# Optimization experiments

Hardware: AMD Instinct MI355X
Metric: run time of the kernel (lower is better)

## Reference

```python
import jax, jax.numpy as jnp
import numpy as np

B, S, E, H = 2, 2048, 1024, 16
D = E // H  # head_dim = 64


def setup_inputs() -> dict:
    key = jax.random.key(0)
    ks = jax.random.split(key, 6)
    scale = 1.0 / np.sqrt(E)
    x = jax.random.normal(ks[0], (B, S, E), dtype=jnp.float32)
    mask = jnp.ones((B, S), dtype=jnp.int32)
    Wqkv = jax.random.normal(ks[1], (E, 3 * E), dtype=jnp.float32) * scale
    bqkv = jax.random.normal(ks[2], (3 * E,), dtype=jnp.float32) * 0.01
    Wout = jax.random.normal(ks[3], (E, E), dtype=jnp.float32) * scale
    bout = jax.random.normal(ks[4], (E,), dtype=jnp.float32) * 0.01
    return {"x": x, "mask": mask, "Wqkv": Wqkv, "bqkv": bqkv, "Wout": Wout, "bout": bout}


def reference(x, mask, Wqkv, bqkv, Wout, bout):
    Bn, Sn, En = x.shape
    qkv = x @ Wqkv + bqkv                      # [B,S,3E]
    qkv = qkv.reshape(Bn, Sn, 3, H, D)
    qkv = jnp.transpose(qkv, (2, 0, 3, 1, 4))  # [3,B,H,S,D]
    q, k, v = qkv[0], qkv[1], qkv[2]
    scores = jnp.einsum('bhqd,bhkd->bhqk', q, k) / np.sqrt(D).astype(np.float32)
    m = mask[:, None, None, :]                 # [B,1,1,S]
    scores = jnp.where(m == 0, jnp.float32(-jnp.inf), scores)
    attn = jax.nn.softmax(scores, axis=-1)
    out = jnp.einsum('bhqk,bhkd->bhqd', attn, v)  # [B,H,S,D]
    out = jnp.transpose(out, (0, 2, 1, 3)).reshape(Bn, Sn, En)
    return out @ Wout + bout
```

## Files before the change

kernel.cpp:

```cpp
#include <hip/hip_runtime.h>


typedef __attribute__((ext_vector_type(8))) short short8;
typedef __attribute__((ext_vector_type(4))) short short4b;
typedef __attribute__((ext_vector_type(4))) float floatx4;
typedef unsigned short ushort_t;

static __device__ __forceinline__ ushort_t f2bf(float f) {
    unsigned u = __float_as_uint(f);
    u += 0x7fffu + ((u >> 16) & 1u);
    return (ushort_t)(u >> 16);
}
static __device__ __forceinline__ float bf2f(ushort_t h) {
    return __uint_as_float(((unsigned)h) << 16);
}
#if __has_builtin(__builtin_amdgcn_cvt_pk_bf16_f32)
typedef __attribute__((ext_vector_type(2))) __bf16 bf16x2_t;
static __device__ __forceinline__ unsigned pack2bf(float a, float b) {
    bf16x2_t r = __builtin_amdgcn_cvt_pk_bf16_f32(a, b);
    return __builtin_bit_cast(unsigned, r);
}
#else
static __device__ __forceinline__ unsigned pack2bf(float a, float b) {
    return (unsigned)f2bf(a) | ((unsigned)f2bf(b) << 16);
}
#endif
static __device__ __forceinline__ float hexp2(float x) {
    return __builtin_amdgcn_exp2f(x);
}
static __device__ __forceinline__ void gload16(const void* g, void* l) {
    __builtin_amdgcn_global_load_lds(
        (const __attribute__((address_space(1))) unsigned int*)g,
        (__attribute__((address_space(3))) unsigned int*)l, 16, 0, 0);
}

static __device__ __forceinline__ floatx4 mfma16(short4b a, short4b b, floatx4 c) {
#if __has_builtin(__builtin_amdgcn_mfma_f32_16x16x16_bf16)
    return __builtin_amdgcn_mfma_f32_16x16x16_bf16(a, b, c, 0, 0, 0);
#elif __has_builtin(__builtin_amdgcn_mfma_f32_16x16x16bf16_1k)
    return __builtin_amdgcn_mfma_f32_16x16x16bf16_1k(a, b, c, 0, 0, 0);
#else
    asm("v_mfma_f32_16x16x16_bf16 %0, %1, %2, %0" : "+v"(c) : "v"(a), "v"(b));
    return c;
#endif
}

__global__ __launch_bounds__(256) void prep(
    const float* __restrict__ x, ushort_t* __restrict__ xb,
    const float* __restrict__ Wqkv, ushort_t* __restrict__ wqT,
    const float* __restrict__ Wout, ushort_t* __restrict__ woT,
    const int* __restrict__ mask, float* __restrict__ maddg)
{
    __shared__ float tile[32][33];
    const int bk = blockIdx.x;
    const int t = threadIdx.x;
    if (bk < 4096) {
        int i = bk * 256 + t;
        float4 v = ((const float4*)x)[i];
        uint2 o;
        o.x = pack2bf(v.x, v.y);
        o.y = pack2bf(v.z, v.w);
        ((uint2*)xb)[i] = o;
        return;
    }
    if (bk < 8192) {
        const float* W; ushort_t* WT; int K, N, id;
        if (bk < 7168) { W = Wqkv; WT = wqT; K = 1024; N = 3072; id = bk - 4096;
                         int nb = (id % 96) * 32, kb = (id / 96) * 32;
                         const int r = t >> 3, c4 = (t & 7) * 4;
                         float4 v = *(const float4*)&W[(size_t)(kb + r) * N + nb + c4];
                         tile[r][c4+0]=v.x; tile[r][c4+1]=v.y; tile[r][c4+2]=v.z; tile[r][c4+3]=v.w;
                         __syncthreads();
                         uint2 o;
                         o.x = pack2bf(tile[c4+0][r], tile[c4+1][r]);
                         o.y = pack2bf(tile[c4+2][r], tile[c4+3][r]);
                         ((uint2*)WT)[((size_t)(nb + r) * K + kb + c4) >> 2] = o;
        } else {         W = Wout; WT = woT; K = 1024; N = 1024; id = bk - 7168;
                         int nb = (id % 32) * 32, kb = (id / 32) * 32;
                         const int r = t >> 3, c4 = (t & 7) * 4;
                         float4 v = *(const float4*)&W[(size_t)(kb + r) * N + nb + c4];
                         tile[r][c4+0]=v.x; tile[r][c4+1]=v.y; tile[r][c4+2]=v.z; tile[r][c4+3]=v.w;
                         __syncthreads();
                         uint2 o;
                         o.x = pack2bf(tile[c4+0][r], tile[c4+1][r]);
                         o.y = pack2bf(tile[c4+2][r], tile[c4+3][r]);
                         ((uint2*)WT)[((size_t)(nb + r) * K + kb + c4) >> 2] = o;
        }
        return;
    }
    {
        int i = (bk - 8192) * 256 + t;
        maddg[i] = (mask[i] ? 0.f : -1e30f) - 24.0f;
    }
}

__global__ __launch_bounds__(256, 3) void gemm_qkv(
    const ushort_t* __restrict__ A, const ushort_t* __restrict__ B,
    const float* __restrict__ bias, ushort_t* __restrict__ qkvb,
    ushort_t* __restrict__ vtg)
{
    const int K = 1024;
    __shared__ ushort_t Ah[128][32], Bh[128][32];
    __shared__ ushort_t Tb[64][136];
    const int bn = blockIdx.x * 128, bm = blockIdx.y * 128;
    const int t = threadIdx.x, w = t >> 6, lane = t & 63;
    const int l15 = lane & 15, quad = lane >> 4;
    const int wm = w >> 1, wn = w & 1;

    const int srow = w * 32 + (lane >> 2);
    const int skp  = (lane & 3) ^ ((lane >> 2) & 3);
    const int scol = skp * 8;
    const ushort_t* ga = A + (size_t)(bm + srow) * K + scol;
    const ushort_t* gb = B + (size_t)(bn + srow) * K + scol;
    const size_t rstep = (size_t)16 * K;
    const int fcol = ((quad ^ (l15 & 3)) * 8);

    floatx4 acc[4][4];
    #pragma unroll
    for (int mt = 0; mt < 4; ++mt)
        #pragma unroll
        for (int nt = 0; nt < 4; ++nt) acc[mt][nt] = (floatx4){0.f, 0.f, 0.f, 0.f};

    for (int k0 = 0; k0 < K; k0 += 32) {
        #pragma unroll
        for (int i = 0; i < 2; ++i) {
            gload16(ga + i * rstep + k0, &Ah[w * 32 + i * 16][0]);
            gload16(gb + i * rstep + k0, &Bh[w * 32 + i * 16][0]);
        }
        __syncthreads();
        short8 ah[4], bh[4];
        #pragma unroll
        for (int x = 0; x < 4; ++x) {
            ah[x] = *(const short8*)&Ah[wm * 64 + x * 16 + l15][fcol];
            bh[x] = *(const short8*)&Bh[wn * 64 + x * 16 + l15][fcol];
        }
        #pragma unroll
        for (int mt = 0; mt < 4; ++mt)
            #pragma unroll
            for (int nt = 0; nt < 4; ++nt)
                acc[mt][nt] = __builtin_amdgcn_mfma_f32_16x16x32_bf16(ah[mt], bh[nt], acc[mt][nt], 0, 0, 0);
        __syncthreads();
    }

    if (bn < 2048) {
        #pragma unroll
        for (int mt = 0; mt < 4; ++mt)
            #pragma unroll
            for (int r = 0; r < 4; ++r) {
                size_t row = (size_t)(bm + wm * 64 + mt * 16 + quad * 4 + r) * 2048;
                #pragma unroll
                for (int nt = 0; nt < 4; ++nt) {
                    int col = bn + wn * 64 + nt * 16 + l15;
                    qkvb[row + col] = f2bf(acc[mt][nt][r] + bias[col]);
                }
            }
    } else {
        const int h0 = (bn - 2048) >> 6;
        const int b  = bm >> 11, s0 = bm & 2047;
        #pragma unroll
        for (int hh = 0; hh < 2; ++hh) {
            if (wn == hh) {
                #pragma unroll
                for (int mt = 0; mt < 4; ++mt)
                    #pragma unroll
                    for (int nt = 0; nt < 4; ++nt) {
                        int d = nt * 16 + l15;
                        int sb = wm * 64 + mt * 16 + quad * 4;
                        float bv = bias[bn + hh * 64 + nt * 16 + l15];
                        uint2 pk;
                        pk.x = pack2bf(acc[mt][nt][0] + bv, acc[mt][nt][1] + bv);
                        pk.y = pack2bf(acc[mt][nt][2] + bv, acc[mt][nt][3] + bv);
                        *(uint2*)&Tb[d][sb] = pk;
                    }
            }
            __syncthreads();
            ushort_t* vbase = vtg + ((size_t)((b * 16 + h0 + hh) * 64)) * 2048 + s0;
            #pragma unroll
            for (int it = 0; it < 4; ++it) {
                int idx = t + it * 256;
                int d = idx >> 4, ch = idx & 15;
                uint4 v = *(const uint4*)&Tb[d][ch * 8];
                *(uint4*)&vbase[(size_t)d * 2048 + ch * 8] = v;
            }
            __syncthreads();
        }
    }
}

__global__ __launch_bounds__(256, 3) void gemm_bf16_f32_64(
    const ushort_t* __restrict__ A, const ushort_t* __restrict__ B,
    const float* __restrict__ bias, float* __restrict__ C,
    int M, int N, int K)
{
    __shared__ ushort_t Ah[64][32], Bh[128][32];
    const int bn = blockIdx.x * 128, bm = blockIdx.y * 64;
    const int t = threadIdx.x, w = t >> 6, lane = t & 63;
    const int l15 = lane & 15, quad = lane >> 4;
    const int wm = w >> 1, wn = w & 1;

    const int srow = w * 16 + (lane >> 2);
    const int skp  = (lane & 3) ^ ((lane >> 2) & 3);
    const int scol = skp * 8;
    const ushort_t* ga  = A + (size_t)(bm + srow) * K + scol;
    const ushort_t* gb0 = B + (size_t)(bn + srow) * K + scol;
    const ushort_t* gb1 = B + (size_t)(bn + 64 + srow) * K + scol;
    const int fcol = ((quad ^ (l15 & 3)) * 8);

    floatx4 acc[2][4];
    #pragma unroll
    for (int mt = 0; mt < 2; ++mt)
        #pragma unroll
        for (int nt = 0; nt < 4; ++nt) acc[mt][nt] = (floatx4){0.f, 0.f, 0.f, 0.f};

    for (int k0 = 0; k0 < K; k0 += 32) {
        gload16(ga  + k0, &Ah[w * 16][0]);
        gload16(gb0 + k0, &Bh[w * 16][0]);
        gload16(gb1 + k0, &Bh[64 + w * 16][0]);
        __syncthreads();
        short8 ah[2], bh[4];
        #pragma unroll
        for (int x = 0; x < 2; ++x)
            ah[x] = *(const short8*)&Ah[wm * 32 + x * 16 + l15][fcol];
        #pragma unroll
        for (int x = 0; x < 4; ++x)
            bh[x] = *(const short8*)&Bh[wn * 64 + x * 16 + l15][fcol];
        #pragma unroll
        for (int mt = 0; mt < 2; ++mt)
            #pragma unroll
            for (int nt = 0; nt < 4; ++nt)
                acc[mt][nt] = __builtin_amdgcn_mfma_f32_16x16x32_bf16(ah[mt], bh[nt], acc[mt][nt], 0, 0, 0);
        __syncthreads();
    }
    #pragma unroll
    for (int mt = 0; mt < 2; ++mt)
        #pragma unroll
        for (int r = 0; r < 4; ++r) {
            size_t row = (size_t)(bm + wm * 32 + mt * 16 + quad * 4 + r) * N;
            #pragma unroll
            for (int nt = 0; nt < 4; ++nt) {
                int col = bn + wn * 64 + nt * 16 + l15;
                C[row + col] = acc[mt][nt][r] + bias[col];
            }
        }
}

__global__ __launch_bounds__(512, 4) void flash_v8(
    const ushort_t* __restrict__ qkv, const ushort_t* __restrict__ vtg,
    const float* __restrict__ maddg, ushort_t* __restrict__ attn)
{
    __shared__ ushort_t Ks[2][64][64];
    __shared__ ushort_t Vt[2][64][64];

    const int blk = blockIdx.x;
    const int xcd = blk & 7, rr = blk >> 3;
    const int qi = rr & 15, g = xcd + 8 * (rr >> 4);
    const int b = g >> 4, h = g & 15, q0 = qi * 128;

    const int t = threadIdx.x, wave = t >> 6, lane = t & 63;
    const int l15 = lane & 15, quad = lane >> 4;
    const size_t bS = (size_t)b * 2048;
    const float c1 = 0.125f * 1.44269504088896340736f;

    short8 qf[2];
    {
        int q = q0 + wave * 16 + l15;
        const ushort_t* qp = qkv + (bS + q) * 2048 + h * 64;
        qf[0] = *(const short8*)(qp + quad * 8);
        qf[1] = *(const short8*)(qp + 32 + quad * 8);
    }

    const int srow  = wave * 8 + (lane >> 3);
    const int schnk = ((lane & 7) ^ ((lane >> 3) & 7)) * 8;
    const ushort_t* gK = qkv + (bS + srow) * 2048 + 1024 + h * 64 + schnk;
    const ushort_t* gV = vtg + ((size_t)(b * 16 + h) * 64 + srow) * 2048 + schnk;
    const float* gM = maddg + b * 2048;

    gload16(gK, &Ks[0][wave * 8][0]);
    gload16(gV, &Vt[0][wave * 8][0]);
    __syncthreads();

    floatx4 outacc[4];
    float lsum = 0.f;
    #pragma unroll
    for (int dt = 0; dt < 4; ++dt) outacc[dt] = (floatx4){0.f, 0.f, 0.f, 0.f};

    int cur = 0;
    for (int kt = 0; kt < 32; ++kt) {
        const int k0 = kt * 64;
        {
            const int kn = (kt + 1 < 32) ? (kt + 1) * 64 : 0;
            const int nb = cur ^ 1;
            gload16(gK + (size_t)kn * 2048, &Ks[nb][wave * 8][0]);
            gload16(gV + kn,                &Vt[nb][wave * 8][0]);
        }
        float4 madd4[4];
        #pragma unroll
        for (int c = 0; c < 4; ++c)
            madd4[c] = *(const float4*)&gM[k0 + c * 16 + quad * 4];

        short8 kf[2][4];
        #pragma unroll
        for (int kc = 0; kc < 2; ++kc)
            #pragma unroll
            for (int c = 0; c < 4; ++c) {
                int ch = ((kc * 4 + quad) ^ (l15 & 7)) * 8;
                kf[kc][c] = *(const short8*)&Ks[cur][c * 16 + l15][ch];
            }
        short4b vA[4][4];
        #pragma unroll
        for (int c = 0; c < 4; ++c) {
            const int vby = (((2 * c + (quad >> 1)) ^ (l15 & 7)) * 16 + (quad & 1) * 8);
            #pragma unroll
            for (int dt = 0; dt < 4; ++dt)
                vA[c][dt] = *(const short4b*)((const char*)&Vt[cur][dt * 16 + l15][0] + vby);
        }

        floatx4 sc[4];
        __builtin_amdgcn_s_setprio(1);
        #pragma unroll
        for (int c = 0; c < 4; ++c) {
            sc[c] = (floatx4){0.f, 0.f, 0.f, 0.f};
            sc[c] = __builtin_amdgcn_mfma_f32_16x16x32_bf16(kf[0][c], qf[0], sc[c], 0, 0, 0);
            sc[c] = __builtin_amdgcn_mfma_f32_16x16x32_bf16(kf[1][c], qf[1], sc[c], 0, 0, 0);
        }
        __builtin_amdgcn_s_setprio(0);
        #pragma unroll
        for (int c = 0; c < 4; ++c) {
            float p0 = hexp2(fmaf(sc[c][0], c1, madd4[c].x));
            float p1 = hexp2(fmaf(sc[c][1], c1, madd4[c].y));
            float p2 = hexp2(fmaf(sc[c][2], c1, madd4[c].z));
            float p3 = hexp2(fmaf(sc[c][3], c1, madd4[c].w));
            lsum += (p0 + p1) + (p2 + p3);
            uint2 u;
            u.x = pack2bf(p0, p1);
            u.y = pack2bf(p2, p3);
            short4b pb = __builtin_bit_cast(short4b, u);
            __builtin_amdgcn_s_setprio(1);
            #pragma unroll
            for (int dt = 0; dt < 4; ++dt)
                outacc[dt] = mfma16(vA[c][dt], pb, outacc[dt]);
            __builtin_amdgcn_s_setprio(0);
        }
        __syncthreads();
        cur ^= 1;
    }

    {
        lsum += __shfl_xor(lsum, 16);
        lsum += __shfl_xor(lsum, 32);
        float inv = 1.f / lsum;
        int q = q0 + wave * 16 + l15;
        ushort_t* orow = attn + (bS + q) * 1024 + h * 64;
        #pragma unroll
        for (int dt = 0; dt < 4; ++dt) {
            uint2 pk;
            pk.x = pack2bf(outacc[dt][0] * inv, outacc[dt][1] * inv);
            pk.y = pack2bf(outacc[dt][2] * inv, outacc[dt][3] * inv);
            *(uint2*)&orow[dt * 16 + quad * 4] = pk;
        }
    }
}

extern "C" void kernel_launch(void* const* d_in, const int* in_sizes, int n_in,
                              void* d_out, int out_size, void* d_ws, size_t ws_size,
                              hipStream_t stream) {
    const float* x    = (const float*)d_in[0];
    const int*   mask = (const int*)  d_in[1];
    const float* Wqkv = (const float*)d_in[2];
    const float* bqkv = (const float*)d_in[3];
    const float* Wout = (const float*)d_in[4];
    const float* bout = (const float*)d_in[5];
    float* out = (float*)d_out;

    char* ws = (char*)d_ws;
    ushort_t* xb    = (ushort_t*)(ws);
    ushort_t* wqT   = (ushort_t*)(ws + 8388608);
    ushort_t* qkvb  = (ushort_t*)(ws + 14680064);
    ushort_t* vtg   = (ushort_t*)(ws + 31457280);
    ushort_t* attnb = (ushort_t*)(ws + 39845888);
    ushort_t* woT   = (ushort_t*)(ws + 48234496);
    float*    maddg = (float*)   (ws + 50331648);

    const int M = 4096, E = 1024, N3 = 3072;

    prep<<<dim3(8208), dim3(256), 0, stream>>>(
        x, xb, Wqkv, wqT, Wout, woT, mask, maddg);

    gemm_qkv<<<dim3(N3 / 128, M / 128), dim3(256), 0, stream>>>(
        xb, wqT, bqkv, qkvb, vtg);

    flash_v8<<<dim3(512), dim3(512), 0, stream>>>(qkvb, vtg, maddg, attnb);

    gemm_bf16_f32_64<<<dim3(E / 128, M / 64), dim3(256), 0, stream>>>(
        attnb, woT, bout, out, M, E, E);
}
```

Measured before the change: 196.8 us.

## Switch flash attention to 32x32x16 MFMA with permlane32 swap for P operand

The attention kernel now uses 32x32x16 bf16 MFMA tiles for both QK^T and PV. Each wave handles 32 queries instead of 16, and the block shrinks from 512 to 256 threads. The score fragments are rearranged into the B-operand layout with permlane32_swap, avoiding an LDS round-trip. K/V fragments are read from LDS inside the MFMA loops rather than preloaded. The larger MFMA tiles should cut instruction count and LDS traffic per FLOP, at the cost of more registers per wave and fewer waves per block.

```diff
diff --git a/kernel.cpp b/kernel.cpp
--- a/kernel.cpp
+++ b/kernel.cpp
@@ -4,6 +4,7 @@
 typedef __attribute__((ext_vector_type(8))) short short8;
 typedef __attribute__((ext_vector_type(4))) short short4b;
 typedef __attribute__((ext_vector_type(4))) float floatx4;
+typedef __attribute__((ext_vector_type(16))) float floatx16;
 typedef unsigned short ushort_t;
 
 static __device__ __forceinline__ ushort_t f2bf(float f) {
@@ -34,16 +35,24 @@
         (__attribute__((address_space(3))) unsigned int*)l, 16, 0, 0);
 }
 
-static __device__ __forceinline__ floatx4 mfma16(short4b a, short4b b, floatx4 c) {
-#if __has_builtin(__builtin_amdgcn_mfma_f32_16x16x16_bf16)
-    return __builtin_amdgcn_mfma_f32_16x16x16_bf16(a, b, c, 0, 0, 0);
-#elif __has_builtin(__builtin_amdgcn_mfma_f32_16x16x16bf16_1k)
-    return __builtin_amdgcn_mfma_f32_16x16x16bf16_1k(a, b, c, 0, 0, 0);
+#if __has_builtin(__builtin_amdgcn_permlane32_swap)
+typedef __attribute__((ext_vector_type(2))) unsigned uint2v_t;
+static __device__ __forceinline__ void plswap(unsigned x, unsigned y,
+                                              unsigned& o0, unsigned& o1) {
+    uint2v_t r = __builtin_amdgcn_permlane32_swap(x, y, false, false);
+    o0 = r.x; o1 = r.y;
+}
 #else
-    asm("v_mfma_f32_16x16x16_bf16 %0, %1, %2, %0" : "+v"(c) : "v"(a), "v"(b));
-    return c;
+static __device__ __forceinline__ void plswap(unsigned x, unsigned y,
+                                              unsigned& o0, unsigned& o1) {
+    int l = (int)(threadIdx.x & 63);
+    bool hi = l >= 32;
+    unsigned xsw = (unsigned)__shfl((int)x, l ^ 32);
+    unsigned ysw = (unsigned)__shfl((int)y, l ^ 32);
+    o0 = hi ? ysw : x;
+    o1 = hi ? y : xsw;
+}
 #endif
-}
 
 __global__ __launch_bounds__(256) void prep(
     const float* __restrict__ x, ushort_t* __restrict__ xb,
@@ -244,7 +253,7 @@
         }
 }
 
-__global__ __launch_bounds__(512, 4) void flash_v8(
+__global__ __launch_bounds__(256, 2) void flash_v10(
     const ushort_t* __restrict__ qkv, const ushort_t* __restrict__ vtg,
     const float* __restrict__ maddg, ushort_t* __restrict__ attn)
 {
@@ -257,32 +266,33 @@
     const int b = g >> 4, h = g & 15, q0 = qi * 128;
 
     const int t = threadIdx.x, wave = t >> 6, lane = t & 63;
-    const int l15 = lane & 15, quad = lane >> 4;
+    const int l31 = lane & 31, hi = lane >> 5, l7 = lane & 7;
     const size_t bS = (size_t)b * 2048;
     const float c1 = 0.125f * 1.44269504088896340736f;
 
-    short8 qf[2];
+    short8 qf[4];
     {
-        int q = q0 + wave * 16 + l15;
-        const ushort_t* qp = qkv + (bS + q) * 2048 + h * 64;
-        qf[0] = *(const short8*)(qp + quad * 8);
-        qf[1] = *(const short8*)(qp + 32 + quad * 8);
-    }
-
-    const int srow  = wave * 8 + (lane >> 3);
+        int q = q0 + wave * 32 + l31;
+        const ushort_t* qp = qkv + (bS + q) * 2048 + h * 64 + hi * 8;
+        #pragma unroll
+        for (int ks = 0; ks < 4; ++ks)
+            qf[ks] = *(const short8*)(qp + ks * 16);
+    }
+
+    const int srow  = wave * 16 + (lane >> 3);
     const int schnk = ((lane & 7) ^ ((lane >> 3) & 7)) * 8;
     const ushort_t* gK = qkv + (bS + srow) * 2048 + 1024 + h * 64 + schnk;
     const ushort_t* gV = vtg + ((size_t)(b * 16 + h) * 64 + srow) * 2048 + schnk;
     const float* gM = maddg + b * 2048;
 
-    gload16(gK, &Ks[0][wave * 8][0]);
-    gload16(gV, &Vt[0][wave * 8][0]);
+    gload16(gK,            &Ks[0][wave * 16][0]);
+    gload16(gK + 8 * 2048, &Ks[0][wave * 16 + 8][0]);
+    gload16(gV,            &Vt[0][wave * 16][0]);
+    gload16(gV + 8 * 2048, &Vt[0][wave * 16 + 8][0]);
     __syncthreads();
 
-    floatx4 outacc[4];
+    floatx16 outacc[2] = {};
     float lsum = 0.f;
-    #pragma unroll
-    for (int dt = 0; dt < 4; ++dt) outacc[dt] = (floatx4){0.f, 0.f, 0.f, 0.f};
 
     int cur = 0;
     for (int kt = 0; kt < 32; ++kt) {
@@ -290,55 +300,59 @@
         {
             const int kn = (kt + 1 < 32) ? (kt + 1) * 64 : 0;
             const int nb = cur ^ 1;
-            gload16(gK + (size_t)kn * 2048, &Ks[nb][wave * 8][0]);
-            gload16(gV + kn,                &Vt[nb][wave * 8][0]);
-        }
-        float4 madd4[4];
-        #pragma unroll
-        for (int c = 0; c < 4; ++c)
-            madd4[c] = *(const float4*)&gM[k0 + c * 16 + quad * 4];
-
-        short8 kf[2][4];
-        #pragma unroll
-        for (int kc = 0; kc < 2; ++kc)
-            #pragma unroll
-            for (int c = 0; c < 4; ++c) {
-                int ch = ((kc * 4 + quad) ^ (l15 & 7)) * 8;
-                kf[kc][c] = *(const short8*)&Ks[cur][c * 16 + l15][ch];
-            }
-        short4b vA[4][4];
-        #pragma unroll
-        for (int c = 0; c < 4; ++c) {
-            const int vby = (((2 * c + (quad >> 1)) ^ (l15 & 7)) * 16 + (quad & 1) * 8);
-            #pragma unroll
-            for (int dt = 0; dt < 4; ++dt)
-                vA[c][dt] = *(const short4b*)((const char*)&Vt[cur][dt * 16 + l15][0] + vby);
-        }
-
-        floatx4 sc[4];
+            gload16(gK + (size_t)kn * 2048,       &Ks[nb][wave * 16][0]);
+            gload16(gK + (size_t)(kn + 8) * 2048, &Ks[nb][wave * 16 + 8][0]);
+            gload16(gV + kn,                      &Vt[nb][wave * 16][0]);
+            gload16(gV + kn + 8 * 2048,           &Vt[nb][wave * 16 + 8][0]);
+        }
+        float4 m4[2][4];
+        #pragma unroll
+        for (int t32 = 0; t32 < 2; ++t32)
+            #pragma unroll
+            for (int gr = 0; gr < 4; ++gr)
+                m4[t32][gr] = *(const float4*)&gM[k0 + t32 * 32 + gr * 8 + hi * 4];
+
+        floatx16 sc[2] = {};
         __builtin_amdgcn_s_setprio(1);
         #pragma unroll
-        for (int c = 0; c < 4; ++c) {
-            sc[c] = (floatx4){0.f, 0.f, 0.f, 0.f};
-            sc[c] = __builtin_amdgcn_mfma_f32_16x16x32_bf16(kf[0][c], qf[0], sc[c], 0, 0, 0);
-            sc[c] = __builtin_amdgcn_mfma_f32_16x16x32_bf16(kf[1][c], qf[1], sc[c], 0, 0, 0);
-        }
+        for (int t32 = 0; t32 < 2; ++t32)
+            #pragma unroll
+            for (int ks = 0; ks < 4; ++ks) {
+                const int ch = ((2 * ks + hi) ^ l7) * 8;
+                short8 ka = *(const short8*)&Ks[cur][t32 * 32 + l31][ch];
+                sc[t32] = __builtin_amdgcn_mfma_f32_32x32x16_bf16(ka, qf[ks], sc[t32], 0, 0, 0);
+            }
         __builtin_amdgcn_s_setprio(0);
-        #pragma unroll
-        for (int c = 0; c < 4; ++c) {
-            float p0 = hexp2(fmaf(sc[c][0], c1, madd4[c].x));
-            float p1 = hexp2(fmaf(sc[c][1], c1, madd4[c].y));
-            float p2 = hexp2(fmaf(sc[c][2], c1, madd4[c].z));
-            float p3 = hexp2(fmaf(sc[c][3], c1, madd4[c].w));
-            lsum += (p0 + p1) + (p2 + p3);
-            uint2 u;
-            u.x = pack2bf(p0, p1);
-            u.y = pack2bf(p2, p3);
-            short4b pb = __builtin_bit_cast(short4b, u);
+
+        unsigned W[2][4][2];
+        #pragma unroll
+        for (int t32 = 0; t32 < 2; ++t32)
+            #pragma unroll
+            for (int gr = 0; gr < 4; ++gr) {
+                float p0 = hexp2(fmaf(sc[t32][gr * 4 + 0], c1, m4[t32][gr].x));
+                float p1 = hexp2(fmaf(sc[t32][gr * 4 + 1], c1, m4[t32][gr].y));
+                float p2 = hexp2(fmaf(sc[t32][gr * 4 + 2], c1, m4[t32][gr].z));
+                float p3 = hexp2(fmaf(sc[t32][gr * 4 + 3], c1, m4[t32][gr].w));
+                lsum += (p0 + p1) + (p2 + p3);
+                W[t32][gr][0] = pack2bf(p0, p1);
+                W[t32][gr][1] = pack2bf(p2, p3);
+            }
+
+        #pragma unroll
+        for (int ks2 = 0; ks2 < 4; ++ks2) {
+            const int t32 = ks2 >> 1;
+            const int ae  = (ks2 & 1) * 2;
+            uint4 u;
+            plswap(W[t32][ae][0], W[t32][ae + 1][0], u.x, u.z);
+            plswap(W[t32][ae][1], W[t32][ae + 1][1], u.y, u.w);
+            short8 pb = __builtin_bit_cast(short8, u);
+            const int ch = ((2 * ks2 + hi) ^ l7) * 8;
             __builtin_amdgcn_s_setprio(1);
             #pragma unroll
-            for (int dt = 0; dt < 4; ++dt)
-                outacc[dt] = mfma16(vA[c][dt], pb, outacc[dt]);
+            for (int dt = 0; dt < 2; ++dt) {
+                short8 va = *(const short8*)&Vt[cur][dt * 32 + l31][ch];
+                outacc[dt] = __builtin_amdgcn_mfma_f32_32x32x16_bf16(va, pb, outacc[dt], 0, 0, 0);
+            }
             __builtin_amdgcn_s_setprio(0);
         }
         __syncthreads();
@@ -346,18 +360,19 @@
     }
 
     {
-        lsum += __shfl_xor(lsum, 16);
         lsum += __shfl_xor(lsum, 32);
         float inv = 1.f / lsum;
-        int q = q0 + wave * 16 + l15;
+        int q = q0 + wave * 32 + l31;
         ushort_t* orow = attn + (bS + q) * 1024 + h * 64;
         #pragma unroll
-        for (int dt = 0; dt < 4; ++dt) {
-            uint2 pk;
-            pk.x = pack2bf(outacc[dt][0] * inv, outacc[dt][1] * inv);
-            pk.y = pack2bf(outacc[dt][2] * inv, outacc[dt][3] * inv);
-            *(uint2*)&orow[dt * 16 + quad * 4] = pk;
-        }
+        for (int dt = 0; dt < 2; ++dt)
+            #pragma unroll
+            for (int gr = 0; gr < 4; ++gr) {
+                uint2 pk;
+                pk.x = pack2bf(outacc[dt][gr * 4 + 0] * inv, outacc[dt][gr * 4 + 1] * inv);
+                pk.y = pack2bf(outacc[dt][gr * 4 + 2] * inv, outacc[dt][gr * 4 + 3] * inv);
+                *(uint2*)&orow[dt * 32 + gr * 8 + hi * 4] = pk;
+            }
     }
 }
 
@@ -389,7 +404,7 @@
     gemm_qkv<<<dim3(N3 / 128, M / 128), dim3(256), 0, stream>>>(
         xb, wqT, bqkv, qkvb, vtg);
 
-    flash_v8<<<dim3(512), dim3(512), 0, stream>>>(qkvb, vtg, maddg, attnb);
+    flash_v10<<<dim3(512), dim3(256), 0, stream>>>(qkvb, vtg, maddg, attnb);
 
     gemm_bf16_f32_64<<<dim3(E / 128, M / 64), dim3(256), 0, stream>>>(
         attnb, woT, bout, out, M, E, E);
```

Measured after the change: 203.0 us. +3.2%, slower.
